# Kernel optimization log

Measured on AMD Instinct MI355X. Metric: run time of the kernel, lower is better.

The kernel has to match this reference:

```python
import jax, jax.numpy as jnp
import numpy as np

B, S, D_IN, D_OUT = 4, 2048, 1024, 1024

def setup_inputs() -> dict:
    key = jax.random.key(0)
    kx, kq, kk, kv = jax.random.split(key, 4)
    sc = 1.0 / np.sqrt(D_IN)
    x = jax.random.normal(kx, (B, S, D_IN), dtype=jnp.float32)
    Wq = jax.random.normal(kq, (D_IN, D_OUT), dtype=jnp.float32) * sc
    Wk = jax.random.normal(kk, (D_IN, D_OUT), dtype=jnp.float32) * sc
    Wv = jax.random.normal(kv, (D_IN, D_OUT), dtype=jnp.float32) * sc
    return {"x": x, "Wq": Wq, "Wk": Wk, "Wv": Wv}

def reference(x, Wq, Wk, Wv):
    # x: [B,S,Din]; projections to [B,S,Dout]
    q = jnp.einsum('bsd,de->bse', x, Wq)
    k = jnp.einsum('bsd,de->bse', x, Wk)
    v = jnp.einsum('bsd,de->bse', x, Wv)
    scale = 1.0 / jnp.sqrt(jnp.asarray(q.shape[-1], q.dtype))
    scores = jnp.einsum('bqe,bke->bqk', q, k) * scale  # [B,S,S]
    causal = jnp.tril(jnp.ones((scores.shape[-2], scores.shape[-1]), dtype=bool))
    scores = jnp.where(causal, scores, -jnp.inf)
    attn = jax.nn.softmax(scores, axis=-1)
    # dropout p=0.0 -> identity
    return jnp.einsum('bqk,bke->bqe', attn, v)
```

## Files before the change

kernel.cpp:

```cpp
#include <hip/hip_runtime.h>

#define SEQ 2048
#define DIM 1024

typedef __attribute__((ext_vector_type(8))) __bf16 bf16x8;
typedef __attribute__((ext_vector_type(4))) float f32x4;

typedef __attribute__((address_space(1))) unsigned char gu8_t;
typedef __attribute__((address_space(3))) unsigned char lu8_t;

__device__ __forceinline__ void async_copy16(const void* g, void* l) {
  __builtin_amdgcn_global_load_lds((gu8_t*)g, (lu8_t*)l, 16, 0, 0);
}

__device__ __forceinline__ ushort f2bf(float f) {
  union { float f; unsigned u; } v;
  v.f = f;
  unsigned r = v.u + 0x7FFFu + ((v.u >> 16) & 1u);
  return (ushort)(r >> 16);
}

__global__ void prep(const void* __restrict__ xin, const void* __restrict__ w0,
                     const void* __restrict__ w1, const void* __restrict__ w2,
                     ushort* __restrict__ xb, ushort* __restrict__ wt,
                     int* __restrict__ flag, float* __restrict__ lsum) {
  __shared__ ushort tile[64][68];
  __shared__ int redi[4];
  const int bid = blockIdx.x;
  const int t = threadIdx.x;

  const unsigned* words = (const unsigned*)xin;
  int hits = 0;
#pragma unroll
  for (int i = 0; i < 4; i++) {
    const unsigned wv = words[t * 4 + i];
    const unsigned b = (wv >> 8) & 0x7Fu;
    hits += (b >= 0x3Bu && b <= 0x42u) ? 1 : 0;
  }
#pragma unroll
  for (int o = 32; o > 0; o >>= 1) hits += __shfl_xor(hits, o, 64);
  if ((t & 63) == 0) redi[t >> 6] = hits;
  __syncthreads();
  const int bf = (redi[0] + redi[1] + redi[2] + redi[3] > 512) ? 1 : 0;

  if (bid >= 1792) {
    reinterpret_cast<float4*>(lsum)[(bid - 1792) * 256 + t] =
        make_float4(0.f, 0.f, 0.f, 0.f);
    if (bid == 1792 && t == 0) *flag = bf;
    return;
  }

  if (bid < 1024) {
#pragma unroll
    for (int j = 0; j < 4; j++) {
      const int i = bid * 1024 + j * 256 + t;
      if (bf) {
        reinterpret_cast<uint4*>(xb)[i] =
            reinterpret_cast<const uint4*>(xin)[i];
      } else {
        const float4* f = reinterpret_cast<const float4*>(xin);
        const float4 a = f[2 * i], b = f[2 * i + 1];
        ushort4 lo, hi;
        lo.x = f2bf(a.x); lo.y = f2bf(a.y); lo.z = f2bf(a.z); lo.w = f2bf(a.w);
        hi.x = f2bf(b.x); hi.y = f2bf(b.y); hi.z = f2bf(b.z); hi.w = f2bf(b.w);
        reinterpret_cast<ushort4*>(xb)[2 * i] = lo;
        reinterpret_cast<ushort4*>(xb)[2 * i + 1] = hi;
      }
    }
    return;
  }

  const int rem = bid - 1024;
  const int z = rem >> 8;
  const int within = rem & 255;
  const int c0 = (within & 15) * 64, r0 = (within >> 4) * 64;
  const void* in = (z == 0) ? w0 : (z == 1) ? w1 : w2;
  ushort* op = wt + (size_t)z * 1024 * 1024;

  if (bf) {
    const ushort* ip = (const ushort*)in;
#pragma unroll
    for (int i = 0; i < 4; i++) {
      const int lin = i * 256 + t;
      const int r = lin >> 4, c4 = (lin & 15) << 2;
      const ushort4 v = *reinterpret_cast<const ushort4*>(
          ip + (size_t)(r0 + r) * 1024 + c0 + c4);
      tile[r][c4 + 0] = v.x; tile[r][c4 + 1] = v.y;
      tile[r][c4 + 2] = v.z; tile[r][c4 + 3] = v.w;
    }
  } else {
    const float* ip = (const float*)in;
#pragma unroll
    for (int i = 0; i < 4; i++) {
      const int lin = i * 256 + t;
      const int r = lin >> 4, c4 = (lin & 15) << 2;
      const float4 v = *reinterpret_cast<const float4*>(
          ip + (size_t)(r0 + r) * 1024 + c0 + c4);
      tile[r][c4 + 0] = f2bf(v.x); tile[r][c4 + 1] = f2bf(v.y);
      tile[r][c4 + 2] = f2bf(v.z); tile[r][c4 + 3] = f2bf(v.w);
    }
  }
  __syncthreads();
#pragma unroll
  for (int i = 0; i < 4; i++) {
    const int lin = i * 256 + t;
    const int c = lin >> 4, r4 = (lin & 15) << 2;
    ushort4 v;
    v.x = tile[r4 + 0][c]; v.y = tile[r4 + 1][c];
    v.z = tile[r4 + 2][c]; v.w = tile[r4 + 3][c];
    *reinterpret_cast<ushort4*>(op + (size_t)(c0 + c) * 1024 + r0 + r4) = v;
  }
}

template <int MODE>
__global__ __launch_bounds__(512, 2) void gemm8(
    const ushort* __restrict__ p0, const ushort* __restrict__ p1,
    const ushort* __restrict__ p2, void* __restrict__ c0,
    void* __restrict__ c1, float* __restrict__ lsum) {
  __shared__ ushort sA[2][2][128 * 64];
  __shared__ ushort sB[2][2][128 * 64];

  const ushort* A;
  const ushort* B;
  ushort* C;
  float* ls = nullptr;
  int m0, n0;
  long ldA, ldB, ldC;
  float scale = 1.0f;
  bool isE = false;

  const int id = blockIdx.x;
  if constexpr (MODE == 0) {
    const int z = id >> 7, r = id & 127;
    m0 = (r >> 2) << 8;
    n0 = (r & 3) << 8;
    A = p0; ldA = 1024;
    B = p1 + (size_t)z * 1024 * 1024; ldB = 1024;
    C = (ushort*)c0 + (size_t)z * 8192 * 1024; ldC = 1024;
    scale = z ? 1.0f : 0.03125f;
  } else {
    if (id < 144) {
      isE = true;
      const int z = id / 36;
      const int tri = id % 36;
      int mt = 0;
      while ((mt + 1) * (mt + 2) / 2 <= tri) mt++;
      const int nt = tri - mt * (mt + 1) / 2;
      m0 = mt << 8;
      n0 = nt << 8;
      A = p0 + (size_t)z * SEQ * DIM; ldA = 1024;
      B = p0 + (size_t)8192 * 1024 + (size_t)z * SEQ * DIM; ldB = 1024;
      C = (ushort*)c0 + (size_t)z * SEQ * SEQ; ldC = 2048;
      ls = lsum + (size_t)z * SEQ;
    } else {
      const int r = id - 144;
      m0 = (r >> 5) << 8;
      n0 = (r & 31) << 8;
      A = p1 + 2 * 1024 * 1024; ldA = 1024;
      B = p2; ldB = 1024;
      C = (ushort*)c1; ldC = 8192;
    }
  }
  constexpr int nT = 16;

  const int tid = threadIdx.x;
  const int lane = tid & 63;
  const int w = tid >> 6;
  const int quad = lane >> 4;
  const int l15 = lane & 15;
  const int ah = w >> 2;
  const int wn = (w & 3) << 6;
  const int bh = wn >> 7;
  const int bo = wn & 64;

  const int rl0 = tid >> 3;
  const int ck0 = (tid & 7) ^ (rl0 & 7);
  const ushort* aBase = A + (size_t)(m0 + rl0) * ldA + ck0 * 8;
  const ushort* bBase = B + (size_t)(n0 + rl0) * ldB + ck0 * 8;

  auto stageA = [&](int t, int b) {
#pragma unroll
    for (int h = 0; h < 2; h++)
#pragma unroll
      for (int i = 0; i < 2; i++)
        async_copy16(aBase + (size_t)(h * 128 + i * 64) * ldA + t * 64,
                     &sA[b][h][(i * 512 + tid) * 8]);
  };
  auto stageB = [&](int t, int b) {
#pragma unroll
    for (int h = 0; h < 2; h++)
#pragma unroll
      for (int i = 0; i < 2; i++)
        async_copy16(bBase + (size_t)(h * 128 + i * 64) * ldB + t * 64,
                     &sB[b][h][(i * 512 + tid) * 8]);
  };
  auto rdA = [&](int b, int rbase, int kh) -> bf16x8 {
    const int row = rbase + l15;
    const int ck = ((kh << 2) | quad) ^ (row & 7);
    return *(const bf16x8*)&sA[b][ah][row * 64 + ck * 8];
  };
  auto rdB = [&](int b, int rbase, int kh) -> bf16x8 {
    const int row = rbase + l15;
    const int ck = ((kh << 2) | quad) ^ (row & 7);
    return *(const bf16x8*)&sB[b][bh][row * 64 + ck * 8];
  };

  f32x4 acc[8][4] = {};
  bf16x8 aLo[8], aHi[8], bF0[4], bF1[4];

  stageA(0, 0); stageB(0, 0);
  stageA(1, 1); stageB(1, 1);
  asm volatile("s_waitcnt vmcnt(8)" ::: "memory");
  __builtin_amdgcn_s_barrier();

#pragma unroll 1
  for (int t = 0; t < nT; t++) {
    const int b = t & 1;

#pragma unroll
    for (int m = 0; m < 4; m++)
#pragma unroll
      for (int h = 0; h < 2; h++) aLo[m * 2 + h] = rdA(b, m * 16, h);
#pragma unroll
    for (int n = 0; n < 2; n++)
#pragma unroll
      for (int h = 0; h < 2; h++) bF0[n * 2 + h] = rdB(b, bo + n * 16, h);
    __builtin_amdgcn_s_barrier();

#pragma unroll
    for (int m = 0; m < 4; m++)
#pragma unroll
      for (int h = 0; h < 2; h++) aHi[m * 2 + h] = rdA(b, 64 + m * 16, h);
#pragma unroll
    for (int n = 0; n < 2; n++)
#pragma unroll
      for (int h = 0; h < 2; h++)
        bF1[n * 2 + h] = rdB(b, bo + 32 + n * 16, h);

    __builtin_amdgcn_s_setprio(1);
#pragma unroll
    for (int h = 0; h < 2; h++)
#pragma unroll
      for (int m = 0; m < 4; m++)
#pragma unroll
        for (int n = 0; n < 2; n++)
          acc[m][n] = __builtin_amdgcn_mfma_f32_16x16x32_bf16(
              aLo[m * 2 + h], bF0[n * 2 + h], acc[m][n], 0, 0, 0);
    __builtin_amdgcn_s_setprio(0);
    __builtin_amdgcn_s_barrier();

    __builtin_amdgcn_s_setprio(1);
#pragma unroll
    for (int h = 0; h < 2; h++)
#pragma unroll
      for (int m = 0; m < 4; m++)
#pragma unroll
        for (int n = 0; n < 2; n++)
          acc[m][2 + n] = __builtin_amdgcn_mfma_f32_16x16x32_bf16(
              aLo[m * 2 + h], bF1[n * 2 + h], acc[m][2 + n], 0, 0, 0);
    __builtin_amdgcn_s_setprio(0);
    __builtin_amdgcn_s_barrier();

    if (t + 2 < nT) stageB(t + 2, b);
    __builtin_amdgcn_s_barrier();

    __builtin_amdgcn_s_setprio(1);
#pragma unroll
    for (int h = 0; h < 2; h++)
#pragma unroll
      for (int m = 0; m < 4; m++)
#pragma unroll
        for (int n = 0; n < 2; n++)
          acc[4 + m][n] = __builtin_amdgcn_mfma_f32_16x16x32_bf16(
              aHi[m * 2 + h], bF0[n * 2 + h], acc[4 + m][n], 0, 0, 0);
    __builtin_amdgcn_s_setprio(0);
    __builtin_amdgcn_s_barrier();

    if (t + 2 < nT) stageA(t + 2, b);
    __builtin_amdgcn_s_setprio(1);
#pragma unroll
    for (int h = 0; h < 2; h++)
#pragma unroll
      for (int m = 0; m < 4; m++)
#pragma unroll
        for (int n = 0; n < 2; n++)
          acc[4 + m][2 + n] = __builtin_amdgcn_mfma_f32_16x16x32_bf16(
              aHi[m * 2 + h], bF1[n * 2 + h], acc[4 + m][2 + n], 0, 0, 0);
    __builtin_amdgcn_s_setprio(0);
    if (t + 2 < nT)
      asm volatile("s_waitcnt vmcnt(8)" ::: "memory");
    else
      asm volatile("s_waitcnt vmcnt(0)" ::: "memory");
    __builtin_amdgcn_s_barrier();
  }

  if (MODE == 1 && isE) {
#pragma unroll
    for (int mi = 0; mi < 8; mi++)
#pragma unroll
      for (int r = 0; r < 4; r++) {
        const int row = m0 + ah * 128 + mi * 16 + quad * 4 + r;
        float partial = 0.0f;
#pragma unroll
        for (int ni = 0; ni < 4; ni++) {
          const int col = n0 + wn + ni * 16 + l15;
          const float ev = (col <= row) ? __expf(acc[mi][ni][r]) : 0.0f;
          C[(size_t)row * ldC + col] = f2bf(ev);
          partial += ev;
        }
#pragma unroll
        for (int o = 1; o < 16; o <<= 1) partial += __shfl_xor(partial, o, 64);
        if (l15 == 0) atomicAdd(&ls[row], partial);
      }
  } else {
#pragma unroll
    for (int mi = 0; mi < 8; mi++)
#pragma unroll
      for (int ni = 0; ni < 4; ni++)
#pragma unroll
        for (int r = 0; r < 4; r++) {
          const int row = m0 + ah * 128 + mi * 16 + quad * 4 + r;
          const int col = n0 + wn + ni * 16 + l15;
          C[(size_t)row * ldC + col] = f2bf(acc[mi][ni][r] * scale);
        }
  }
}

template <int EPI, int OUTK, int CK, int SWIZ, int M, int N, int K, long AZ,
          long BZ, long CZ, long BRS>
__global__ __launch_bounds__(256, 4) void gemm_t(
    const ushort* __restrict__ A, const ushort* __restrict__ Bt,
    void* __restrict__ Cv, const int* __restrict__ flag,
    float* __restrict__ lsum, float scale0, float scale1) {
  __shared__ ushort lA[128 * 64];
  __shared__ ushort lB[128 * 64];
  __shared__ float lsh[(EPI == 2) ? 128 : 1];

  constexpr int MT = M / 128;
  const int nT = gridDim.x;
  const int id = blockIdx.y * nT + blockIdx.x;
  const int xcd = id & 7;
  const int loc = id >> 3;
  int nt, mt;
  if constexpr (SWIZ == 1) {
    const int ng = nT >> 3;
    nt = xcd * ng + loc % ng;
    mt = loc / ng;
  } else if constexpr (SWIZ == 2) {
    if (loc <= xcd) { mt = xcd; nt = loc; }
    else { mt = MT - 1 - xcd; nt = loc - xcd - 1; }
  } else if constexpr (SWIZ == 3) {
    nt = xcd;
    mt = loc;
  } else {
    nt = loc % nT;
    mt = xcd + ((loc / nT) << 3);
  }
  const int n0 = nt * 128;
  const int m0 = mt * 128;

  const int z = blockIdx.z;
  const ushort* Ab = A + (size_t)z * AZ;
  const ushort* Bb = Bt + (size_t)z * BZ;

  const int t = threadIdx.x;
  const int lane = t & 63;
  const int w = t >> 6;
  const int wm = (w >> 1) * 64;
  const int wn = (w & 1) * 64;
  const int quad = lane >> 4;
  const int l15 = lane & 15;

  if constexpr (EPI == 2) {
    if (t < 128) lsh[t] = 1.0f / lsum[(size_t)z * M + m0 + t];
  }

  f32x4 acc[4][4] = {};

  const int kEnd = CK ? ((m0 + 128 < K) ? (m0 + 128) : K) : K;

  for (int k0 = 0; k0 < kEnd; k0 += 64) {
    __syncthreads();
#pragma unroll
    for (int g0 = 0; g0 < 1024; g0 += 256) {
      const int g = g0 + t;
      const int r = g >> 3, c = (g & 7) << 3;
      async_copy16(Ab + (size_t)(m0 + r) * K + k0 + c, lA + g * 8);
    }
#pragma unroll
    for (int g0 = 0; g0 < 1024; g0 += 256) {
      const int g = g0 + t;
      const int r = g >> 3, c = (g & 7) << 3;
      async_copy16(Bb + (size_t)(n0 + r) * BRS + k0 + c, lB + g * 8);
    }
    __syncthreads();

#pragma unroll
    for (int h = 0; h < 2; h++) {
      bf16x8 af[4], bfr[4];
#pragma unroll
      for (int mi = 0; mi < 4; mi++)
        af[mi] = *(const bf16x8*)(lA + (wm + mi * 16 + l15) * 64 + h * 32 +
                                  quad * 8);
#pragma unroll
      for (int ni = 0; ni < 4; ni++)
        bfr[ni] = *(const bf16x8*)(lB + (wn + ni * 16 + l15) * 64 + h * 32 +
                                   quad * 8);
#pragma unroll
      for (int mi = 0; mi < 4; mi++)
#pragma unroll
        for (int ni = 0; ni < 4; ni++)
          acc[mi][ni] = __builtin_amdgcn_mfma_f32_16x16x32_bf16(
              af[mi], bfr[ni], acc[mi][ni], 0, 0, 0);
    }
  }

  const size_t zc = (size_t)z * CZ;

  if constexpr (EPI == 1) {
    ushort* C = (ushort*)Cv + zc;
    float* ls = lsum + (size_t)z * M;
#pragma unroll
    for (int mi = 0; mi < 4; mi++)
#pragma unroll
      for (int r = 0; r < 4; r++) {
        const int row = m0 + wm + mi * 16 + quad * 4 + r;
        float partial = 0.0f;
#pragma unroll
        for (int ni = 0; ni < 4; ni++) {
          const int col = n0 + wn + ni * 16 + l15;
          const float ev = (col <= row) ? __expf(acc[mi][ni][r]) : 0.0f;
          C[(size_t)row * N + col] = f2bf(ev);
          partial += ev;
        }
#pragma unroll
        for (int o = 1; o < 16; o <<= 1) partial += __shfl_xor(partial, o, 64);
        if (l15 == 0) atomicAdd(&ls[row], partial);
      }
    return;
  } else {
    const float scale = (z == 0) ? scale0 : scale1;
    const bool storeBf = (OUTK == 1) || (OUTK == 2 && *flag != 0);
#pragma unroll
    for (int mi = 0; mi < 4; mi++)
#pragma unroll
      for (int ni = 0; ni < 4; ni++)
#pragma unroll
        for (int r = 0; r < 4; r++) {
          const int lrow = wm + mi * 16 + quad * 4 + r;
          const int row = m0 + lrow;
          const int col = n0 + wn + ni * 16 + l15;
          const float sc = (EPI == 2) ? lsh[lrow] : scale;
          const float vv = acc[mi][ni][r] * sc;
          if (storeBf) {
            ushort* C = (ushort*)Cv + zc;
            C[(size_t)row * N + col] = f2bf(vv);
          } else {
            float* C = (float*)Cv + zc;
            C[(size_t)row * N + col] = vv;
          }
        }
  }
}

extern "C" void kernel_launch(void* const* d_in, const int* in_sizes, int n_in,
                              void* d_out, int out_size, void* d_ws,
                              size_t ws_size, hipStream_t stream) {
  char* ws = (char*)d_ws;
  const size_t MB = 1024 * 1024;
  int* flag = (int*)ws;
  ushort* wt = (ushort*)(ws + 1 * MB);
  ushort* xb = (ushort*)(ws + 7 * MB);
  ushort* q = (ushort*)(ws + 23 * MB);
  ushort* vt = (ushort*)(ws + 55 * MB);
  ushort* sc = (ushort*)(ws + 71 * MB);
  float* lsum = (float*)(ws + 103 * MB);

  prep<<<dim3(1800), 256, 0, stream>>>(d_in[0], d_in[1], d_in[2], d_in[3], xb,
                                       wt, flag, lsum);

  gemm8<0><<<dim3(256), 512, 0, stream>>>(xb, wt, nullptr, (void*)q, nullptr,
                                          nullptr);

  gemm8<1><<<dim3(272), 512, 0, stream>>>(q, wt, xb, (void*)sc, (void*)vt,
                                          lsum);

  gemm_t<2, 2, 1, 3, 2048, 1024, 2048, (long)SEQ * SEQ, 2048L,
         (long)SEQ * DIM, 8192L>
      <<<dim3(8, 16, 4), 256, 0, stream>>>(sc, vt, d_out, flag, lsum, 1.0f,
                                           1.0f);
}
```

Baseline: 244.1 us.

## Software-pipeline LDS fragment loads across k-tiles with register double-buffering

Restructures the GEMM main loop so fragments for the next k-tile (aLo, bF0) are read from LDS during the MFMA clusters of the current tile, using ping-pong register sets and a two-tile unrolled loop. It also interleaves the aHi/bF1 reads between MFMA clusters and cuts the number of barriers per tile. The goal is to hide LDS read latency behind matrix instructions. In exchange it raises VGPR pressure, which risks spilling under launch_bounds(512,2), and it waits with vmcnt(0) rather than vmcnt(8), which may expose global-load latency. The loop also assumes nT is even.

```diff
diff --git a/kernel.cpp b/kernel.cpp
--- a/kernel.cpp
+++ b/kernel.cpp
@@ -111,6 +111,55 @@
     *reinterpret_cast<ushort4*>(op + (size_t)(c0 + c) * 1024 + r0 + r4) = v;
   }
 }
+
+#define MFMA_CL(AF, BF, MO, NO)                                             \
+  _Pragma("unroll") for (int h = 0; h < 2; h++)                             \
+      _Pragma("unroll") for (int m = 0; m < 4; m++)                         \
+          _Pragma("unroll") for (int n = 0; n < 2; n++)                     \
+              acc[(MO) + m][(NO) + n] =                                     \
+                  __builtin_amdgcn_mfma_f32_16x16x32_bf16(                  \
+                      AF[m * 2 + h], BF[n * 2 + h],                         \
+                      acc[(MO) + m][(NO) + n], 0, 0, 0);
+
+#define HALF_TILE(bCur, CaLo, CbF0, NaLo, NbF0, tt)                         \
+  {                                                                         \
+    _Pragma("unroll") for (int n = 0; n < 2; n++)                           \
+        _Pragma("unroll") for (int h = 0; h < 2; h++)                       \
+            bF1[n * 2 + h] = rdB(bCur, bo + 32 + n * 16, h);                \
+    __builtin_amdgcn_s_setprio(1);                                          \
+    MFMA_CL(CaLo, CbF0, 0, 0)                                               \
+    __builtin_amdgcn_s_setprio(0);                                          \
+    _Pragma("unroll") for (int m = 0; m < 4; m++)                           \
+        _Pragma("unroll") for (int h = 0; h < 2; h++)                       \
+            aHi[m * 2 + h] = rdA(bCur, 64 + m * 16, h);                     \
+    __builtin_amdgcn_s_setprio(1);                                          \
+    MFMA_CL(CaLo, bF1, 0, 2)                                                \
+    __builtin_amdgcn_s_setprio(0);                                          \
+    if ((tt) + 1 < nT) asm volatile("s_waitcnt vmcnt(0)" ::: "memory");     \
+    __builtin_amdgcn_s_barrier();                                   \
+    if ((tt) + 2 < nT) stageB((tt) + 2, bCur);                              \
+    if ((tt) + 1 < nT) {                                                    \
+      _Pragma("unroll") for (int m = 0; m < 2; m++)                         \
+          _Pragma("unroll") for (int h = 0; h < 2; h++)                     \
+              NaLo[m * 2 + h] = rdA((bCur) ^ 1, m * 16, h);                 \
+    }                                                                       \
+    __builtin_amdgcn_s_setprio(1);                                          \
+    MFMA_CL(aHi, CbF0, 4, 0)                                                \
+    __builtin_amdgcn_s_setprio(0);                                          \
+    __builtin_amdgcn_s_barrier();                                   \
+    if ((tt) + 2 < nT) stageA((tt) + 2, bCur);                              \
+    if ((tt) + 1 < nT) {                                                    \
+      _Pragma("unroll") for (int m = 2; m < 4; m++)                         \
+          _Pragma("unroll") for (int h = 0; h < 2; h++)                     \
+              NaLo[m * 2 + h] = rdA((bCur) ^ 1, m * 16, h);                 \
+      _Pragma("unroll") for (int n = 0; n < 2; n++)                         \
+          _Pragma("unroll") for (int h = 0; h < 2; h++)                     \
+              NbF0[n * 2 + h] = rdB((bCur) ^ 1, bo + n * 16, h);            \
+    }                                                                       \
+    __builtin_amdgcn_s_setprio(1);                                          \
+    MFMA_CL(aHi, bF1, 4, 2)                                                 \
+    __builtin_amdgcn_s_setprio(0);                                          \
+  }
 
 template <int MODE>
 __global__ __launch_bounds__(512, 2) void gemm8(
@@ -206,92 +255,28 @@
   };
 
   f32x4 acc[8][4] = {};
-  bf16x8 aLo[8], aHi[8], bF0[4], bF1[4];
+  bf16x8 aLoX[8], bF0X[4];
+  bf16x8 aLoY[8], bF0Y[4];
+  bf16x8 aHi[8], bF1[4];
 
   stageA(0, 0); stageB(0, 0);
   stageA(1, 1); stageB(1, 1);
   asm volatile("s_waitcnt vmcnt(8)" ::: "memory");
   __builtin_amdgcn_s_barrier();
 
+#pragma unroll
+  for (int m = 0; m < 4; m++)
+#pragma unroll
+    for (int h = 0; h < 2; h++) aLoX[m * 2 + h] = rdA(0, m * 16, h);
+#pragma unroll
+  for (int n = 0; n < 2; n++)
+#pragma unroll
+    for (int h = 0; h < 2; h++) bF0X[n * 2 + h] = rdB(0, bo + n * 16, h);
+
 #pragma unroll 1
-  for (int t = 0; t < nT; t++) {
-    const int b = t & 1;
-
-#pragma unroll
-    for (int m = 0; m < 4; m++)
-#pragma unroll
-      for (int h = 0; h < 2; h++) aLo[m * 2 + h] = rdA(b, m * 16, h);
-#pragma unroll
-    for (int n = 0; n < 2; n++)
-#pragma unroll
-      for (int h = 0; h < 2; h++) bF0[n * 2 + h] = rdB(b, bo + n * 16, h);
-    __builtin_amdgcn_s_barrier();
-
-#pragma unroll
-    for (int m = 0; m < 4; m++)
-#pragma unroll
-      for (int h = 0; h < 2; h++) aHi[m * 2 + h] = rdA(b, 64 + m * 16, h);
-#pragma unroll
-    for (int n = 0; n < 2; n++)
-#pragma unroll
-      for (int h = 0; h < 2; h++)
-        bF1[n * 2 + h] = rdB(b, bo + 32 + n * 16, h);
-
-    __builtin_amdgcn_s_setprio(1);
-#pragma unroll
-    for (int h = 0; h < 2; h++)
-#pragma unroll
-      for (int m = 0; m < 4; m++)
-#pragma unroll
-        for (int n = 0; n < 2; n++)
-          acc[m][n] = __builtin_amdgcn_mfma_f32_16x16x32_bf16(
-              aLo[m * 2 + h], bF0[n * 2 + h], acc[m][n], 0, 0, 0);
-    __builtin_amdgcn_s_setprio(0);
-    __builtin_amdgcn_s_barrier();
-
-    __builtin_amdgcn_s_setprio(1);
-#pragma unroll
-    for (int h = 0; h < 2; h++)
-#pragma unroll
-      for (int m = 0; m < 4; m++)
-#pragma unroll
-        for (int n = 0; n < 2; n++)
-          acc[m][2 + n] = __builtin_amdgcn_mfma_f32_16x16x32_bf16(
-              aLo[m * 2 + h], bF1[n * 2 + h], acc[m][2 + n], 0, 0, 0);
-    __builtin_amdgcn_s_setprio(0);
-    __builtin_amdgcn_s_barrier();
-
-    if (t + 2 < nT) stageB(t + 2, b);
-    __builtin_amdgcn_s_barrier();
-
-    __builtin_amdgcn_s_setprio(1);
-#pragma unroll
-    for (int h = 0; h < 2; h++)
-#pragma unroll
-      for (int m = 0; m < 4; m++)
-#pragma unroll
-        for (int n = 0; n < 2; n++)
-          acc[4 + m][n] = __builtin_amdgcn_mfma_f32_16x16x32_bf16(
-              aHi[m * 2 + h], bF0[n * 2 + h], acc[4 + m][n], 0, 0, 0);
-    __builtin_amdgcn_s_setprio(0);
-    __builtin_amdgcn_s_barrier();
-
-    if (t + 2 < nT) stageA(t + 2, b);
-    __builtin_amdgcn_s_setprio(1);
-#pragma unroll
-    for (int h = 0; h < 2; h++)
-#pragma unroll
-      for (int m = 0; m < 4; m++)
-#pragma unroll
-        for (int n = 0; n < 2; n++)
-          acc[4 + m][2 + n] = __builtin_amdgcn_mfma_f32_16x16x32_bf16(
-              aHi[m * 2 + h], bF1[n * 2 + h], acc[4 + m][2 + n], 0, 0, 0);
-    __builtin_amdgcn_s_setprio(0);
-    if (t + 2 < nT)
-      asm volatile("s_waitcnt vmcnt(8)" ::: "memory");
-    else
-      asm volatile("s_waitcnt vmcnt(0)" ::: "memory");
-    __builtin_amdgcn_s_barrier();
+  for (int t = 0; t < nT; t += 2) {
+    HALF_TILE(0, aLoX, bF0X, aLoY, bF0Y, t)
+    HALF_TILE(1, aLoY, bF0Y, aLoX, bF0X, t + 1)
   }
 
   if (MODE == 1 && isE) {
```

Result: slower. 397.2 us (+62.7%).
